# Kernel optimization log

Measured on AMD Instinct MI355X. Metric: run time of the kernel, lower is better.

## Reference

```python
import jax, jax.numpy as jnp
import numpy as np

B, L, H, C = 8, 2048, 1024, 64

def setup_inputs() -> dict:
    key = jax.random.key(0)
    k1, k2, k3 = jax.random.split(key, 3)
    feature = jax.random.normal(k1, (B, L, H), dtype=jnp.float32)
    fc_weight = jax.random.normal(k2, (1, H), dtype=jnp.float32) * 0.02
    fc_bias = jnp.zeros((1,), dtype=jnp.float32)
    # (src, end) spans per notebook cell; sort last axis so src <= end
    position_list = jnp.sort(jax.random.randint(k3, (B, C, 2), 0, L, dtype=jnp.int32), axis=-1)
    return {"feature": feature, "fc_weight": fc_weight, "fc_bias": fc_bias,
            "position_list": position_list}


def reference(feature, fc_weight, fc_bias, position_list):
    # feature: [B, L, H]; position_list: [B, C, 2] with (src, end) inclusive spans.
    src = position_list[..., 0]            # [B, C]
    end = position_list[..., 1]            # [B, C]
    pos = jnp.arange(L, dtype=position_list.dtype)  # [L]
    # span membership mask: [B, C, L]
    mask = ((pos[None, None, :] >= src[:, :, None]) &
            (pos[None, None, :] <= end[:, :, None])).astype(feature.dtype)
    counts = jnp.maximum(mask.sum(axis=-1, keepdims=True), 1.0)  # [B, C, 1]
    # mean pooling over each span: segment sum via masked contraction
    pooled = jnp.einsum('bcl,blh->bch', mask, feature) / counts  # [B, C, H]
    # fc: Linear(H, 1)
    logits = jnp.einsum('bch,oh->bco', pooled, fc_weight) + fc_bias  # [B, C, 1]
    # original concatenates per-cell logits in order -> [B*C, 1]
    return logits.reshape(B * C, 1)
```

## Files before the change

kernel.cpp:

```cpp
#include <hip/hip_runtime.h>

#define PB 8
#define PL 2048
#define PH 1024
#define PC 64

__global__ __launch_bounds__(256) void row_dot_kernel(
    const float* __restrict__ feature,
    const float* __restrict__ w,
    float* __restrict__ s)
{
    const int gtid = blockIdx.x * 256 + threadIdx.x;
    const int row  = gtid >> 6;
    const int lane = threadIdx.x & 63;

    const float* rp = feature + (size_t)row * PH;

    float acc = 0.0f;
#pragma unroll
    for (int j = 0; j < PH / 256; ++j) {
        const int idx = j * 256 + lane * 4;
        float4 f = *reinterpret_cast<const float4*>(rp + idx);
        float4 g = *reinterpret_cast<const float4*>(w + idx);
        acc += f.x * g.x + f.y * g.y + f.z * g.z + f.w * g.w;
    }

#pragma unroll
    for (int off = 32; off > 0; off >>= 1)
        acc += __shfl_down(acc, off, 64);

    if (lane == 0) s[row] = acc;
}

__global__ __launch_bounds__(256) void span_pool_kernel(
    const float* __restrict__ s,
    const int* __restrict__ pos,
    const float* __restrict__ bias,
    float* __restrict__ out)
{
    const int gtid = blockIdx.x * 256 + threadIdx.x;
    const int span = gtid >> 6;
    const int lane = threadIdx.x & 63;

    const int b   = span / PC;
    const int src = pos[span * 2 + 0];
    const int end = pos[span * 2 + 1];

    const float* sb = s + b * PL;
    float acc = 0.0f;
    for (int l = src + lane; l <= end; l += 64)
        acc += sb[l];

#pragma unroll
    for (int off = 32; off > 0; off >>= 1)
        acc += __shfl_down(acc, off, 64);

    if (lane == 0) {
        const float cnt = (float)(end - src + 1);
        out[span] = acc / cnt + bias[0];
    }
}

extern "C" void kernel_launch(void* const* d_in, const int* in_sizes, int n_in,
                              void* d_out, int out_size, void* d_ws, size_t ws_size,
                              hipStream_t stream) {
    const float* feature = (const float*)d_in[0];
    const float* fc_w    = (const float*)d_in[1];
    const float* fc_b    = (const float*)d_in[2];
    const int*   pos     = (const int*)d_in[3];
    float*       out     = (float*)d_out;
    float*       s       = (float*)d_ws;

    row_dot_kernel<<<(PB * PL) / 4, 256, 0, stream>>>(feature, fc_w, s);

    span_pool_kernel<<<(PB * PC * 64) / 256, 256, 0, stream>>>(s, pos, fc_b, out);
}
```

Measured before the change: 98.51 us.

## Fuse row-dot and span-pool into one cooperative persistent kernel with grid sync

Merges the two kernels into a single cooperative launch of 1024 blocks, each wave handling several rows in a grid-stride pattern. The fc weight slice is held in registers across those rows instead of being reloaded per row. A grid-wide barrier separates the row-dot phase from the span-pooling phase, removing one kernel launch and the gap between launches. In exchange it adds grid-sync overhead and lowers parallelism per row, and the launch depends on cooperative-launch support and co-residency of all blocks.

```diff
diff --git a/kernel.cpp b/kernel.cpp
--- a/kernel.cpp
+++ b/kernel.cpp
@@ -1,63 +1,75 @@
 #include <hip/hip_runtime.h>
+#include <hip/hip_cooperative_groups.h>
+
+namespace cg = cooperative_groups;
 
 #define PB 8
 #define PL 2048
 #define PH 1024
 #define PC 64
+#define NROWS (PB * PL)
+#define NSPANS (PB * PC)
 
-__global__ __launch_bounds__(256) void row_dot_kernel(
+#define GRID_BLOCKS 1024
+#define BLOCK_THREADS 256
+#define NWAVES (GRID_BLOCKS * (BLOCK_THREADS / 64))
+#define ROWS_PER_WAVE (NROWS / NWAVES)
+
+__global__ __launch_bounds__(BLOCK_THREADS) void fused_kernel(
     const float* __restrict__ feature,
     const float* __restrict__ w,
+    const float* __restrict__ bias,
+    const int* __restrict__ pos,
+    float* __restrict__ out,
     float* __restrict__ s)
 {
-    const int gtid = blockIdx.x * 256 + threadIdx.x;
-    const int row  = gtid >> 6;
+    cg::grid_group grid = cg::this_grid();
+
+    const int wid  = blockIdx.x * (BLOCK_THREADS / 64) + (threadIdx.x >> 6);
     const int lane = threadIdx.x & 63;
 
-    const float* rp = feature + (size_t)row * PH;
+    float4 wf[PH / 256];
+#pragma unroll
+    for (int j = 0; j < PH / 256; ++j)
+        wf[j] = *reinterpret_cast<const float4*>(w + j * 256 + lane * 4);
 
-    float acc = 0.0f;
 #pragma unroll
-    for (int j = 0; j < PH / 256; ++j) {
-        const int idx = j * 256 + lane * 4;
-        float4 f = *reinterpret_cast<const float4*>(rp + idx);
-        float4 g = *reinterpret_cast<const float4*>(w + idx);
-        acc += f.x * g.x + f.y * g.y + f.z * g.z + f.w * g.w;
+    for (int r = 0; r < ROWS_PER_WAVE; ++r) {
+        const int row = wid + r * NWAVES;
+        const float* rp = feature + (size_t)row * PH;
+        float acc = 0.0f;
+#pragma unroll
+        for (int j = 0; j < PH / 256; ++j) {
+            float4 f = *reinterpret_cast<const float4*>(rp + j * 256 + lane * 4);
+            acc += f.x * wf[j].x + f.y * wf[j].y + f.z * wf[j].z + f.w * wf[j].w;
+        }
+#pragma unroll
+        for (int off = 32; off > 0; off >>= 1)
+            acc += __shfl_down(acc, off, 64);
+        if (lane == 0) s[row] = acc;
     }
 
+    __threadfence();
+    grid.sync();
+
+    if (wid < NSPANS) {
+        const int span = wid;
+        const int b    = span >> 6;
+        const int src  = pos[span * 2 + 0];
+        const int end  = pos[span * 2 + 1];
+        const float* sb = s + b * PL;
+
+        float acc = 0.0f;
+        for (int l = src + lane; l <= end; l += 64)
+            acc += sb[l];
 #pragma unroll
-    for (int off = 32; off > 0; off >>= 1)
-        acc += __shfl_down(acc, off, 64);
+        for (int off = 32; off > 0; off >>= 1)
+            acc += __shfl_down(acc, off, 64);
 
-    if (lane == 0) s[row] = acc;
-}
-
-__global__ __launch_bounds__(256) void span_pool_kernel(
-    const float* __restrict__ s,
-    const int* __restrict__ pos,
-    const float* __restrict__ bias,
-    float* __restrict__ out)
-{
-    const int gtid = blockIdx.x * 256 + threadIdx.x;
-    const int span = gtid >> 6;
-    const int lane = threadIdx.x & 63;
-
-    const int b   = span / PC;
-    const int src = pos[span * 2 + 0];
-    const int end = pos[span * 2 + 1];
-
-    const float* sb = s + b * PL;
-    float acc = 0.0f;
-    for (int l = src + lane; l <= end; l += 64)
-        acc += sb[l];
-
-#pragma unroll
-    for (int off = 32; off > 0; off >>= 1)
-        acc += __shfl_down(acc, off, 64);
-
-    if (lane == 0) {
-        const float cnt = (float)(end - src + 1);
-        out[span] = acc / cnt + bias[0];
+        if (lane == 0) {
+            const float cnt = (float)(end - src + 1);
+            out[span] = acc / cnt + bias[0];
+        }
     }
 }
 
@@ -71,7 +83,9 @@
     float*       out     = (float*)d_out;
     float*       s       = (float*)d_ws;
 
-    row_dot_kernel<<<(PB * PL) / 4, 256, 0, stream>>>(feature, fc_w, s);
-
-    span_pool_kernel<<<(PB * PC * 64) / 256, 256, 0, stream>>>(s, pos, fc_b, out);
+    void* args[] = { (void*)&feature, (void*)&fc_w, (void*)&fc_b,
+                     (void*)&pos, (void*)&out, (void*)&s };
+    hipLaunchCooperativeKernel((const void*)fused_kernel,
+                               dim3(GRID_BLOCKS), dim3(BLOCK_THREADS),
+                               args, 0, stream);
 }
```

After: 276.7 us. +180.8%, slower.

## Fuse row dot and span pooling into one kernel with atomic scatter

Applied to the files above, without the earlier changes.

Merges the two kernels. Each wave computes one row's dot product with the fc weight, then each of its 64 lanes checks whether that row falls inside its span and atomically adds the row score divided by the span count into the output. The bias is added once, by the span's first row. This drops the intermediate score buffer and the second kernel launch, at the cost of a memset launch, many float atomics on 512 outputs, and order-dependent rounding in the sums.

```diff
diff --git a/kernel.cpp b/kernel.cpp
--- a/kernel.cpp
+++ b/kernel.cpp
@@ -4,15 +4,19 @@
 #define PL 2048
 #define PH 1024
 #define PC 64
+#define NROWS (PB * PL)
 
-__global__ __launch_bounds__(256) void row_dot_kernel(
+__global__ __launch_bounds__(256) void fused_rowdot_scatter(
     const float* __restrict__ feature,
     const float* __restrict__ w,
-    float* __restrict__ s)
+    const float* __restrict__ bias,
+    const int2* __restrict__ pos,
+    float* __restrict__ out)
 {
-    const int gtid = blockIdx.x * 256 + threadIdx.x;
-    const int row  = gtid >> 6;
+    const int row  = blockIdx.x * 4 + (threadIdx.x >> 6);
     const int lane = threadIdx.x & 63;
+    const int b    = row >> 11;
+    const int l    = row & (PL - 1);
 
     const float* rp = feature + (size_t)row * PH;
 
@@ -26,38 +30,15 @@
     }
 
 #pragma unroll
-    for (int off = 32; off > 0; off >>= 1)
-        acc += __shfl_down(acc, off, 64);
+    for (int m = 1; m < 64; m <<= 1)
+        acc += __shfl_xor(acc, m, 64);
 
-    if (lane == 0) s[row] = acc;
-}
-
-__global__ __launch_bounds__(256) void span_pool_kernel(
-    const float* __restrict__ s,
-    const int* __restrict__ pos,
-    const float* __restrict__ bias,
-    float* __restrict__ out)
-{
-    const int gtid = blockIdx.x * 256 + threadIdx.x;
-    const int span = gtid >> 6;
-    const int lane = threadIdx.x & 63;
-
-    const int b   = span / PC;
-    const int src = pos[span * 2 + 0];
-    const int end = pos[span * 2 + 1];
-
-    const float* sb = s + b * PL;
-    float acc = 0.0f;
-    for (int l = src + lane; l <= end; l += 64)
-        acc += sb[l];
-
-#pragma unroll
-    for (int off = 32; off > 0; off >>= 1)
-        acc += __shfl_down(acc, off, 64);
-
-    if (lane == 0) {
-        const float cnt = (float)(end - src + 1);
-        out[span] = acc / cnt + bias[0];
+    const int2 se = pos[b * PC + lane];
+    if (l >= se.x && l <= se.y) {
+        const float cnt = (float)(se.y - se.x + 1);
+        float v = acc / cnt;
+        if (l == se.x) v += bias[0];
+        atomicAdd(&out[b * PC + lane], v);
     }
 }
 
@@ -67,11 +48,10 @@
     const float* feature = (const float*)d_in[0];
     const float* fc_w    = (const float*)d_in[1];
     const float* fc_b    = (const float*)d_in[2];
-    const int*   pos     = (const int*)d_in[3];
+    const int2*  pos     = (const int2*)d_in[3];
     float*       out     = (float*)d_out;
-    float*       s       = (float*)d_ws;
 
-    row_dot_kernel<<<(PB * PL) / 4, 256, 0, stream>>>(feature, fc_w, s);
+    hipMemsetAsync(out, 0, PB * PC * sizeof(float), stream);
 
-    span_pool_kernel<<<(PB * PC * 64) / 256, 256, 0, stream>>>(s, pos, fc_b, out);
+    fused_rowdot_scatter<<<NROWS / 4, 256, 0, stream>>>(feature, fc_w, fc_b, pos, out);
 }
```

Result: slower. 168.0 us (+70.6%).
